# Optimization experiments

Measured on AMD Instinct MI355X. Metric: run time of the kernel, lower is better.

The kernel has to match this reference:

```python
import jax, jax.numpy as jnp
import numpy as np

H, W = 480, 640
TREF = 1.0        # reference timestamp (events warped to end of window)
TS_SCALING = 1.0  # width of timestamp normalization window
# 4 bilinear corner offsets (dy, dx): top-left, top-right, bottom-left, bottom-right
OFFS = np.array([[0.0, 0.0], [0.0, 1.0], [1.0, 0.0], [1.0, 1.0]], dtype=np.float32)


def setup_inputs() -> dict:
    key = jax.random.key(0)
    k1, k2, k3, k4, k5 = jax.random.split(key, 5)
    B, N = 4, 300000
    flow = jax.random.normal(k1, (B, 2, H, W), jnp.float32) * 2.0  # (x, y) flow maps
    ts = jax.random.uniform(k2, (B, N, 1), jnp.float32)            # event timestamps in [0,1]
    ev_y = jax.random.randint(k3, (B, N), 0, H)
    ev_x = jax.random.randint(k4, (B, N), 0, W)
    pol = jax.random.randint(k5, (B, N), 0, 2)                     # 1 = positive, 0 = negative
    return {"flow": flow, "ts": ts, "ev_y": ev_y, "ev_x": ev_x, "pol": pol}


def _corners(ev):
    """ev: [B,N,2] float (y,x) -> idx [B,4,N,2] corner coords, w [B,4,N] bilinear weights.
    Mirrors get_interpolation(): 4 integer corners, weights clamp(1-|d|,0,1) per axis."""
    base = jnp.floor(ev)[:, None, :, :]                      # [B,1,N,2]
    idx = base + jnp.asarray(OFFS)[None, :, None, :]          # [B,4,N,2]
    w = jnp.prod(jnp.clip(1.0 - jnp.abs(ev[:, None, :, :] - idx), 0.0, 1.0), axis=-1)
    return idx, w


def _splat(idx, w, pol_mask):
    """Mirrors interpolate(): masked bilinear scatter-add into a [B,1,H,W] image.
    idx: [B,4,N,2], w: [B,4,N], pol_mask: [B,1,N] (broadcast over 4 corners)."""
    B = idx.shape[0]
    inb = ((idx[..., 0] >= 0) & (idx[..., 0] <= H - 1) &
           (idx[..., 1] >= 0) & (idx[..., 1] <= W - 1)).astype(w.dtype)
    iy = jnp.clip(idx[..., 0], 0, H - 1).astype(jnp.int32)
    ix = jnp.clip(idx[..., 1], 0, W - 1).astype(jnp.int32)
    flat = (iy * W + ix).reshape(B, -1)                       # [B,4N]
    vals = (w * pol_mask * inb).reshape(B, -1)                # [B,4N]
    img = jnp.zeros((B, H * W), w.dtype).at[jnp.arange(B)[:, None], flat].add(vals)
    return img.reshape(B, 1, H, W)


def _sample(fmap, locs):
    """Mirrors get_event_flow(): bilinear gather of fmap [B,H,W] at float locs [B,N,2] (y,x)."""
    B = fmap.shape[0]
    idx, w = _corners(locs)
    inb = ((idx[..., 0] >= 0) & (idx[..., 0] <= H - 1) &
           (idx[..., 1] >= 0) & (idx[..., 1] <= W - 1)).astype(w.dtype)
    iy = jnp.clip(idx[..., 0], 0, H - 1).astype(jnp.int32)
    ix = jnp.clip(idx[..., 1], 0, W - 1).astype(jnp.int32)
    vals = fmap[jnp.arange(B)[:, None, None], iy, ix] * w * inb   # [B,4,N]
    return vals.sum(axis=1)                                        # [B,N]


def reference(flow, ts, ev_y, ev_x, pol):
    # event pixel locations (y, x)
    loc = jnp.stack([ev_y.astype(flow.dtype), ev_x.astype(flow.dtype)], axis=-1)  # [B,N,2]
    # gather per-event flow (flow channel 0 = x, channel 1 = y)
    fx = _sample(flow[:, 0], loc)   # [B,N]
    fy = _sample(flow[:, 1], loc)   # [B,N]
    # linear forward warp to tref
    dt = TREF - ts[..., 0]                                           # [B,N]
    warped = loc + dt[..., None] * jnp.stack([fy, fx], axis=-1)      # [B,N,2] (y,x)
    # iwe_formatting: bilinear splat of counts and normalized timestamps per polarity
    idx, w = _corners(warped)
    norm_ts = 1.0 - jnp.abs(TREF - ts[..., 0]) / TS_SCALING          # [B,N]
    pm_pos = (pol == 1).astype(w.dtype)[:, None, :]                  # [B,1,N]
    pm_neg = (pol == 0).astype(w.dtype)[:, None, :]
    iwe_pos = _splat(idx, w, pm_pos)
    iwe_neg = _splat(idx, w, pm_neg)
    wt = w * norm_ts[:, None, :]
    iwe_pos_ts = _splat(idx, wt, pm_pos)
    iwe_neg_ts = _splat(idx, wt, pm_neg)
    # [B,4,H,W]: (iwe_pos, iwe_neg, iwe_pos_ts, iwe_neg_ts)
    return jnp.concatenate([iwe_pos, iwe_neg, iwe_pos_ts, iwe_neg_ts], axis=1)
```

## Files before the change

kernel.cpp:

```cpp
#include <hip/hip_runtime.h>


#define IMG_H 480
#define IMG_W 640

#define OT_H 32
#define OT_W 32
#define OTY (IMG_H / OT_H)
#define OTX (IMG_W / OT_W)
#define OT_PER_B (OTY * OTX)
#define NB 4
#define NT (NB * OT_PER_B)

#define ACC_PLANE (OT_H * OT_W)

#define CURS_STRIDE 16
#define WS_CURS 0
#define WS_SPILLCNT 76800
#define WS_SPILL 81920
#define SPILL_CAP 32768
#define WS_RECS 606208

#define K1_THREADS 256
#define K1_IPT 8
#define K1_CHUNK (K1_THREADS * K1_IPT)

#define DUP_INVALID 0xFFFFFFFFu

#define QSCALE 1024.0f
#define INV_QSCALE 9.765625e-04f

#define Q20 1048576.0f
#define INV_Q20 9.5367431640625e-07f

__global__ void __launch_bounds__(K1_THREADS)
warp_scatter_kernel(const float* __restrict__ flow, const float* __restrict__ ts,
                    const int* __restrict__ ev_y, const int* __restrict__ ev_x,
                    const int* __restrict__ pol,
                    unsigned* __restrict__ dcurs, unsigned* __restrict__ spillcnt,
                    float4* __restrict__ spill, uint2* __restrict__ drecs,
                    int N, int cap, int nchunk) {
    __shared__ unsigned lh[OT_PER_B];
    __shared__ unsigned lbase[OT_PER_B];
    const int tid = threadIdx.x;
    const int L = blockIdx.x;
    const int b = (L >> 1) & 3;
    const int chunk = (L >> 3) * 2 + (L & 1);
    if (chunk >= nchunk) return;
    const int base = chunk * K1_CHUNK;

    for (int j = tid; j < OT_PER_B; j += K1_THREADS) lh[j] = 0;

    int   eyK[K1_IPT], exK[K1_IPT], poK[K1_IPT];
    float tsK[K1_IPT];
    bool  vK[K1_IPT];
    #pragma unroll
    for (int k = 0; k < K1_IPT; ++k) {
        const int idx = base + k * K1_THREADS + tid;
        vK[k] = (idx < N);
        const int i = b * N + (vK[k] ? idx : 0);
        eyK[k] = ev_y[i];
        exK[k] = ev_x[i];
        tsK[k] = ts[i];
        poK[k] = pol[i];
    }

    const float* fb = flow + (size_t)b * 2 * IMG_H * IMG_W;
    float fxK[K1_IPT], fyK[K1_IPT];
    #pragma unroll
    for (int k = 0; k < K1_IPT; ++k) {
        const int pix = eyK[k] * IMG_W + exK[k];
        fxK[k] = fb[pix];
        fyK[k] = fb[IMG_H * IMG_W + pix];
    }

    __syncthreads();

    float wyK[K1_IPT], wxK[K1_IPT];
    unsigned metaK[K1_IPT];
    unsigned dupS[K1_IPT][4];

    #pragma unroll
    for (int k = 0; k < K1_IPT; ++k) {
        float wy = 0.f, wx = 0.f;
        unsigned meta = 0;
        unsigned d0 = DUP_INVALID, d1 = DUP_INVALID,
                 d2 = DUP_INVALID, d3 = DUP_INVALID;
        if (vK[k]) {
            const float t = tsK[k];
            const float dt = 1.0f - t;
            wy = (float)eyK[k] + dt * fyK[k];
            wx = (float)exK[k] + dt * fxK[k];
            const float nts = 1.0f - fabsf(1.0f - t);
            const int p = poK[k] & 1;
            int qt = __float2int_rn(nts * 32767.0f);
            qt = min(max(qt, 0), 32767);
            meta = (unsigned)qt | ((unsigned)p << 15);

            const int iy0 = (int)floorf(wy);
            const int ix0 = (int)floorf(wx);
            const int ry0 = iy0 >> 5;
            const int ry1 = (iy0 + 1) >> 5;
            const bool cy0 = (iy0 >= 0) && (iy0 < IMG_H);
            const bool cy1 = (iy0 + 1 >= 0) && (iy0 + 1 < IMG_H)
                             && (!cy0 || ry1 != ry0);
            const int rx0 = ix0 >> 5;
            const int rx1 = (ix0 + 1) >> 5;
            const bool cx0 = (ix0 >= 0) && (ix0 < IMG_W);
            const bool cx1 = (ix0 + 1 >= 0) && (ix0 + 1 < IMG_W)
                             && (!cx0 || rx1 != rx0);

            if (cy0 && cx0) {
                const unsigned lt = (unsigned)(ry0 * OTX + rx0);
                d0 = (lt << 16) | atomicAdd(&lh[lt], 1u);
            }
            if (cy0 && cx1) {
                const unsigned lt = (unsigned)(ry0 * OTX + rx1);
                d1 = (lt << 16) | atomicAdd(&lh[lt], 1u);
            }
            if (cy1 && cx0) {
                const unsigned lt = (unsigned)(ry1 * OTX + rx0);
                d2 = (lt << 16) | atomicAdd(&lh[lt], 1u);
            }
            if (cy1 && cx1) {
                const unsigned lt = (unsigned)(ry1 * OTX + rx1);
                d3 = (lt << 16) | atomicAdd(&lh[lt], 1u);
            }
        }
        wyK[k] = wy; wxK[k] = wx; metaK[k] = meta;
        dupS[k][0] = d0; dupS[k][1] = d1; dupS[k][2] = d2; dupS[k][3] = d3;
    }
    __syncthreads();

    for (int j = tid; j < OT_PER_B; j += K1_THREADS) {
        const unsigned n = lh[j];
        lbase[j] = n ? atomicAdd(&dcurs[(size_t)(b * OT_PER_B + j) * CURS_STRIDE], n)
                     : 0u;
    }
    __syncthreads();

    #pragma unroll
    for (int k = 0; k < K1_IPT; ++k) {
        #pragma unroll
        for (int d = 0; d < 4; ++d) {
            const unsigned dp = dupS[k][d];
            if (dp == DUP_INVALID) continue;
            const unsigned lt = dp >> 16;
            const unsigned rk = dp & 0xFFFFu;
            const int dty = (int)(lt / OTX);
            const int dtx = (int)(lt % OTX);
            const unsigned slot = lbase[lt] + rk;
            if (slot < (unsigned)cap) {
                int qy = __float2int_rn((wyK[k] - 32.0f * dty + 1.0f) * QSCALE);
                int qx = __float2int_rn((wxK[k] - 32.0f * dtx + 1.0f) * QSCALE);
                qy = min(max(qy, 0), 65535);
                qx = min(max(qx, 0), 65535);
                uint2 dr;
                dr.x = (unsigned)qy | ((unsigned)qx << 16);
                dr.y = metaK[k];
                drecs[(size_t)(b * OT_PER_B + lt) * cap + slot] = dr;
            } else {
                const unsigned g = atomicAdd(spillcnt, 1u);
                if (g < SPILL_CAP) {
                    float4 s;
                    s.x = wyK[k]; s.y = wxK[k];
                    s.z = (float)(metaK[k] & 0x7FFFu) * (1.0f / 32767.0f);
                    s.w = __uint_as_float(0x80000000u
                            | (unsigned)((b << 1) | (metaK[k] >> 15))
                            | ((unsigned)dty << 8) | ((unsigned)dtx << 16));
                    spill[g] = s;
                }
            }
        }
    }
}

__device__ __forceinline__ void
splat_rec(unsigned rx_, unsigned ry_, unsigned long long* __restrict__ acc64) {
    const float ry  = (float)(rx_ & 0xFFFFu) * INV_QSCALE - 1.0f;
    const float rx  = (float)(rx_ >> 16)     * INV_QSCALE - 1.0f;
    const float nts = (float)(ry_ & 0x7FFFu) * (1.0f / 32767.0f);
    const int p = (int)((ry_ >> 15) & 1u);
    const float byf = floorf(ry), bxf = floorf(rx);
    const int iy0 = (int)byf, ix0 = (int)bxf;
    const float ay = ry - byf, ax = rx - bxf;
    const float wyv[2] = {1.0f - ay, ay};
    const float wxv[2] = {1.0f - ax, ax};
    unsigned long long* accp = acc64 + (p ? 0 : 1) * ACC_PLANE;
    #pragma unroll
    for (int dy = 0; dy < 2; ++dy) {
        const int gy = iy0 + dy;
        if ((unsigned)gy >= (unsigned)OT_H) continue;
        #pragma unroll
        for (int dx = 0; dx < 2; ++dx) {
            const int gx = ix0 + dx;
            if ((unsigned)gx >= (unsigned)OT_W) continue;
            const float w = wyv[dy] * wxv[dx];
            const unsigned qw  = __float2uint_rn(w * Q20);
            const unsigned qwt = __float2uint_rn(w * nts * Q20);
            atomicAdd(&accp[gy * OT_W + gx],
                      ((unsigned long long)qwt << 32) | (unsigned long long)qw);
        }
    }
}

__global__ void __launch_bounds__(256)
splat_kernel(const uint2* __restrict__ drecs, const unsigned* __restrict__ dcurs,
             const float4* __restrict__ spill, const unsigned* __restrict__ spillcnt,
             float* __restrict__ out, int cap) {
    __shared__ unsigned long long acc64[2 * ACC_PLANE];
    const int L = blockIdx.x;
    const int myb = (L >> 1) & 3;
    const int rb  = (L >> 3) * 2 + (L & 1);
    const int tile = myb * OT_PER_B + rb;
    const int tid = threadIdx.x;
    #pragma unroll
    for (int j = tid; j < 2 * ACC_PLANE; j += 256) acc64[j] = 0ull;
    __syncthreads();

    const int sy  = rb / OTX;
    const int sx  = rb % OTX;

    const unsigned cnt = min(dcurs[(size_t)tile * CURS_STRIDE], (unsigned)cap);
    const uint2* recs = drecs + (size_t)tile * cap;
    const uint4* base4 = (const uint4*)recs;
    const unsigned npair = cnt >> 1;
    for (unsigned u = tid; u < npair; u += 256) {
        const uint4 q = base4[u];
        splat_rec(q.x, q.y, acc64);
        splat_rec(q.z, q.w, acc64);
    }
    if ((cnt & 1u) && tid == 0) {
        const uint2 r = recs[cnt - 1];
        splat_rec(r.x, r.y, acc64);
    }

    const unsigned nsp = min(*spillcnt, (unsigned)SPILL_CAP);
    for (unsigned i = tid; i < nsp; i += 256) {
        const float4 s = spill[i];
        const unsigned meta = __float_as_uint(s.w);
        if ((int)((meta >> 1) & 3u) != myb) continue;
        if (meta & 0x80000000u) {
            if ((int)((meta >> 8) & 31u) != sy || (int)((meta >> 16) & 31u) != sx)
                continue;
        }
        const int p = (int)(meta & 1u);
        const float wy = s.x, wx = s.y, nts = s.z;
        const float byf = floorf(wy), bxf = floorf(wx);
        const int iy0 = (int)byf, ix0 = (int)bxf;
        const float ay = wy - byf, ax = wx - bxf;
        const float wyv[2] = {1.0f - ay, ay};
        const float wxv[2] = {1.0f - ax, ax};
        unsigned long long* accp = acc64 + (p ? 0 : 1) * ACC_PLANE;
        #pragma unroll
        for (int dy = 0; dy < 2; ++dy) {
            const int gy = iy0 + dy;
            if ((gy >> 5) != sy) continue;
            #pragma unroll
            for (int dx = 0; dx < 2; ++dx) {
                const int gx = ix0 + dx;
                if ((gx >> 5) != sx) continue;
                const float w = wyv[dy] * wxv[dx];
                const unsigned qw  = __float2uint_rn(w * Q20);
                const unsigned qwt = __float2uint_rn(w * nts * Q20);
                atomicAdd(&accp[(gy & 31) * OT_W + (gx & 31)],
                          ((unsigned long long)qwt << 32) | (unsigned long long)qw);
            }
        }
    }
    __syncthreads();

    const int y0 = sy * OT_H;
    const int x0 = sx * OT_W;
    float* outb = out + (size_t)myb * 4 * IMG_H * IMG_W;
    for (int q = tid; q < 2 * (ACC_PLANE / 4); q += 256) {
        const int pl  = q / (ACC_PLANE / 4);
        const int rem = q % (ACC_PLANE / 4);
        const int ry  = rem / (OT_W / 4);
        const int rx4 = rem % (OT_W / 4);
        float4 c4, t4;
        const unsigned long long* cell = acc64 + pl * ACC_PLANE + rem * 4;
        float* c = &c4.x; float* t = &t4.x;
        #pragma unroll
        for (int j = 0; j < 4; ++j) {
            const unsigned long long v = cell[j];
            c[j] = (float)(unsigned)(v & 0xFFFFFFFFull) * INV_Q20;
            t[j] = (float)(unsigned)(v >> 32) * INV_Q20;
        }
        const size_t off = (size_t)(y0 + ry) * IMG_W + x0 + rx4 * 4;
        *(float4*)(outb + (size_t)pl * IMG_H * IMG_W + off) = c4;
        *(float4*)(outb + (size_t)(pl + 2) * IMG_H * IMG_W + off) = t4;
    }
}

__device__ __forceinline__ void
warp_from(const float* __restrict__ flow, int b, int y, int x, float t,
          float& wy, float& wx, float& nts) {
    const float* fb = flow + (size_t)b * 2 * IMG_H * IMG_W;
    const int pix = y * IMG_W + x;
    const float fx = fb[pix];
    const float fy = fb[IMG_H * IMG_W + pix];
    const float dt = 1.0f - t;
    wy = (float)y + dt * fy;
    wx = (float)x + dt * fx;
    nts = 1.0f - fabsf(1.0f - t);
}

__global__ void __launch_bounds__(256)
event_splat_fallback(const float* __restrict__ flow, const float* __restrict__ ts,
                     const int* __restrict__ ev_y, const int* __restrict__ ev_x,
                     const int* __restrict__ pol, float* __restrict__ out,
                     int N, int total) {
    const int i = blockIdx.x * blockDim.x + threadIdx.x;
    if (i >= total) return;
    const int b = i / N;
    float wy, wx, nts;
    warp_from(flow, b, ev_y[i], ev_x[i], ts[i], wy, wx, nts);
    const int p = pol[i];
    const float byf = floorf(wy), bxf = floorf(wx);
    const int iy0 = (int)byf, ix0 = (int)bxf;
    const float ay = wy - byf, ax = wx - bxf;
    const float wyv[2] = {1.0f - ay, ay};
    const float wxv[2] = {1.0f - ax, ax};
    float* out_c = out + ((size_t)b * 4 + (p ? 0 : 1)) * IMG_H * IMG_W;
    float* out_t = out_c + 2 * IMG_H * IMG_W;
    #pragma unroll
    for (int dy = 0; dy < 2; ++dy) {
        const int gy = iy0 + dy;
        if (gy < 0 || gy >= IMG_H) continue;
        #pragma unroll
        for (int dx = 0; dx < 2; ++dx) {
            const int gx = ix0 + dx;
            if (gx < 0 || gx >= IMG_W) continue;
            const float w = wyv[dy] * wxv[dx];
            const int o = gy * IMG_W + gx;
            atomicAdd(out_c + o, w);
            atomicAdd(out_t + o, w * nts);
        }
    }
}

extern "C" void kernel_launch(void* const* d_in, const int* in_sizes, int n_in,
                              void* d_out, int out_size, void* d_ws, size_t ws_size,
                              hipStream_t stream) {
    const float* flow = (const float*)d_in[0];
    const float* ts   = (const float*)d_in[1];
    const int*   ev_y = (const int*)d_in[2];
    const int*   ev_x = (const int*)d_in[3];
    const int*   pol  = (const int*)d_in[4];
    float* out = (float*)d_out;

    const int total = in_sizes[2];
    const int B = out_size / (4 * IMG_H * IMG_W);
    const int N = total / B;
    char* ws = (char*)d_ws;

    int cap = 0;
    if (ws_size > (size_t)WS_RECS)
        cap = (int)((ws_size - WS_RECS) / ((size_t)NT * 8));
    if (cap > 4096) cap = 4096;
    cap &= ~3;

    if (B == NB && cap >= 1280) {
        unsigned* dcurs    = (unsigned*)(ws + WS_CURS);
        unsigned* spillcnt = (unsigned*)(ws + WS_SPILLCNT);
        float4*   spill    = (float4*)(ws + WS_SPILL);
        uint2*    drecs    = (uint2*)(ws + WS_RECS);

        hipMemsetAsync(ws, 0, WS_SPILL, stream);

        const int nchunk = (N + K1_CHUNK - 1) / K1_CHUNK;
        const int g1 = 8 * ((nchunk + 1) / 2);
        warp_scatter_kernel<<<g1, K1_THREADS, 0, stream>>>(
            flow, ts, ev_y, ev_x, pol, dcurs, spillcnt, spill, drecs,
            N, cap, nchunk);
        splat_kernel<<<NT, 256, 0, stream>>>(drecs, dcurs, spill, spillcnt,
                                             out, cap);
        return;
    }

    hipMemsetAsync(d_out, 0, (size_t)out_size * sizeof(float), stream);
    const int blocks = (total + 255) / 256;
    event_splat_fallback<<<blocks, 256, 0, stream>>>(flow, ts, ev_y, ev_x, pol,
                                                     out, N, total);
}
```

Baseline: 119.1 us.

## Fuse warp-scatter and splat passes into one cooperative kernel with grid sync

The two-kernel pipeline (event warp/bin scatter, then per-tile splat) becomes a single cooperative launch of 1024 blocks. A grid-wide sync separates the phases, and blocks then loop over the 1200 output tiles. The aim is to remove the second kernel launch and the gap between kernels. In exchange it adds grid-sync cost and a residency requirement (256 threads, 4 blocks per CU via launch bounds). Tiles no longer map one-to-one to blocks, so some blocks process two tiles serially. The old two-kernel path remains as a fallback if cooperative launch is unavailable or fails.

```diff
diff --git a/kernel.cpp b/kernel.cpp
--- a/kernel.cpp
+++ b/kernel.cpp
@@ -1,4 +1,7 @@
 #include <hip/hip_runtime.h>
+#include <hip/hip_cooperative_groups.h>
+
+namespace cg = cooperative_groups;
 
 
 #define IMG_H 480
@@ -25,6 +28,8 @@
 #define K1_IPT 8
 #define K1_CHUNK (K1_THREADS * K1_IPT)
 
+#define COOP_GRID 1024
+
 #define DUP_INVALID 0xFFFFFFFFu
 
 #define QSCALE 1024.0f
@@ -33,20 +38,14 @@
 #define Q20 1048576.0f
 #define INV_Q20 9.5367431640625e-07f
 
-__global__ void __launch_bounds__(K1_THREADS)
-warp_scatter_kernel(const float* __restrict__ flow, const float* __restrict__ ts,
-                    const int* __restrict__ ev_y, const int* __restrict__ ev_x,
-                    const int* __restrict__ pol,
-                    unsigned* __restrict__ dcurs, unsigned* __restrict__ spillcnt,
-                    float4* __restrict__ spill, uint2* __restrict__ drecs,
-                    int N, int cap, int nchunk) {
-    __shared__ unsigned lh[OT_PER_B];
-    __shared__ unsigned lbase[OT_PER_B];
-    const int tid = threadIdx.x;
-    const int L = blockIdx.x;
-    const int b = (L >> 1) & 3;
-    const int chunk = (L >> 3) * 2 + (L & 1);
-    if (chunk >= nchunk) return;
+__device__ __forceinline__ void
+k1_phase(const float* __restrict__ flow, const float* __restrict__ ts,
+         const int* __restrict__ ev_y, const int* __restrict__ ev_x,
+         const int* __restrict__ pol,
+         unsigned* __restrict__ dcurs, unsigned* __restrict__ spillcnt,
+         float4* __restrict__ spill, uint2* __restrict__ drecs,
+         int N, int cap, int b, int chunk, int tid,
+         unsigned* __restrict__ lh, unsigned* __restrict__ lbase) {
     const int base = chunk * K1_CHUNK;
 
     for (int j = tid; j < OT_PER_B; j += K1_THREADS) lh[j] = 0;
@@ -204,17 +203,15 @@
     }
 }
 
-__global__ void __launch_bounds__(256)
-splat_kernel(const uint2* __restrict__ drecs, const unsigned* __restrict__ dcurs,
-             const float4* __restrict__ spill, const unsigned* __restrict__ spillcnt,
-             float* __restrict__ out, int cap) {
-    __shared__ unsigned long long acc64[2 * ACC_PLANE];
-    const int L = blockIdx.x;
-    const int myb = (L >> 1) & 3;
-    const int rb  = (L >> 3) * 2 + (L & 1);
+__device__ __forceinline__ void
+k2_tile(const uint2* __restrict__ drecs, const unsigned* __restrict__ dcurs,
+        const float4* __restrict__ spill, const unsigned* __restrict__ spillcnt,
+        float* __restrict__ out, int cap, int t, int tid,
+        unsigned long long* __restrict__ acc64) {
+    const int myb = (t >> 1) & 3;
+    const int rb  = (t >> 3) * 2 + (t & 1);
     const int tile = myb * OT_PER_B + rb;
-    const int tid = threadIdx.x;
-    #pragma unroll
+
     for (int j = tid; j < 2 * ACC_PLANE; j += 256) acc64[j] = 0ull;
     __syncthreads();
 
@@ -280,17 +277,73 @@
         const int rx4 = rem % (OT_W / 4);
         float4 c4, t4;
         const unsigned long long* cell = acc64 + pl * ACC_PLANE + rem * 4;
-        float* c = &c4.x; float* t = &t4.x;
+        float* c = &c4.x; float* tt = &t4.x;
         #pragma unroll
         for (int j = 0; j < 4; ++j) {
             const unsigned long long v = cell[j];
-            c[j] = (float)(unsigned)(v & 0xFFFFFFFFull) * INV_Q20;
-            t[j] = (float)(unsigned)(v >> 32) * INV_Q20;
+            c[j]  = (float)(unsigned)(v & 0xFFFFFFFFull) * INV_Q20;
+            tt[j] = (float)(unsigned)(v >> 32) * INV_Q20;
         }
         const size_t off = (size_t)(y0 + ry) * IMG_W + x0 + rx4 * 4;
         *(float4*)(outb + (size_t)pl * IMG_H * IMG_W + off) = c4;
         *(float4*)(outb + (size_t)(pl + 2) * IMG_H * IMG_W + off) = t4;
     }
+    __syncthreads();
+}
+
+__global__ void __launch_bounds__(256, 4)
+fused_warp_splat(const float* __restrict__ flow, const float* __restrict__ ts,
+                 const int* __restrict__ ev_y, const int* __restrict__ ev_x,
+                 const int* __restrict__ pol,
+                 unsigned* __restrict__ dcurs, unsigned* __restrict__ spillcnt,
+                 float4* __restrict__ spill, uint2* __restrict__ drecs,
+                 float* __restrict__ out, int N, int cap, int nchunk) {
+    __shared__ unsigned long long acc64[2 * ACC_PLANE];
+    unsigned* lh    = (unsigned*)acc64;
+    unsigned* lbase = lh + OT_PER_B;
+
+    const int tid = threadIdx.x;
+    const int L = blockIdx.x;
+    const int b = (L >> 1) & 3;
+    const int chunk = (L >> 3) * 2 + (L & 1);
+
+    if (chunk < nchunk) {
+        k1_phase(flow, ts, ev_y, ev_x, pol, dcurs, spillcnt, spill, drecs,
+                 N, cap, b, chunk, tid, lh, lbase);
+    }
+
+    __threadfence();
+    cg::this_grid().sync();
+
+    for (int t = L; t < NT; t += (int)gridDim.x)
+        k2_tile(drecs, dcurs, spill, spillcnt, out, cap, t, tid, acc64);
+}
+
+__global__ void __launch_bounds__(K1_THREADS)
+warp_scatter_kernel(const float* __restrict__ flow, const float* __restrict__ ts,
+                    const int* __restrict__ ev_y, const int* __restrict__ ev_x,
+                    const int* __restrict__ pol,
+                    unsigned* __restrict__ dcurs, unsigned* __restrict__ spillcnt,
+                    float4* __restrict__ spill, uint2* __restrict__ drecs,
+                    int N, int cap, int nchunk) {
+    __shared__ unsigned lh[OT_PER_B];
+    __shared__ unsigned lbase[OT_PER_B];
+    const int tid = threadIdx.x;
+    const int L = blockIdx.x;
+    const int b = (L >> 1) & 3;
+    const int chunk = (L >> 3) * 2 + (L & 1);
+    if (chunk >= nchunk) return;
+    k1_phase(flow, ts, ev_y, ev_x, pol, dcurs, spillcnt, spill, drecs,
+             N, cap, b, chunk, tid, lh, lbase);
+}
+
+__global__ void __launch_bounds__(256)
+splat_kernel(const uint2* __restrict__ drecs, const unsigned* __restrict__ dcurs,
+             const float4* __restrict__ spill, const unsigned* __restrict__ spillcnt,
+             float* __restrict__ out, int cap) {
+    __shared__ unsigned long long acc64[2 * ACC_PLANE];
+    k2_tile(drecs, dcurs, spill, spillcnt, out, cap, blockIdx.x, threadIdx.x,
+            acc64);
 }
 
 __device__ __forceinline__ void
@@ -370,12 +423,34 @@
         hipMemsetAsync(ws, 0, WS_SPILL, stream);
 
         const int nchunk = (N + K1_CHUNK - 1) / K1_CHUNK;
-        const int g1 = 8 * ((nchunk + 1) / 2);
-        warp_scatter_kernel<<<g1, K1_THREADS, 0, stream>>>(
-            flow, ts, ev_y, ev_x, pol, dcurs, spillcnt, spill, drecs,
-            N, cap, nchunk);
-        splat_kernel<<<NT, 256, 0, stream>>>(drecs, dcurs, spill, spillcnt,
-                                             out, cap);
+
+        bool fused_ok = false;
+        {
+            int coop = 0, dev = 0;
+            if (hipGetDevice(&dev) == hipSuccess &&
+                hipDeviceGetAttribute(&coop, hipDeviceAttributeCooperativeLaunch,
+                                      dev) == hipSuccess && coop) {
+                void* args[] = {(void*)&flow, (void*)&ts, (void*)&ev_y,
+                                (void*)&ev_x, (void*)&pol, (void*)&dcurs,
+                                (void*)&spillcnt, (void*)&spill, (void*)&drecs,
+                                (void*)&out, (void*)&N, (void*)&cap,
+                                (void*)&nchunk};
+                if (hipLaunchCooperativeKernel((void*)fused_warp_splat,
+                                               dim3(COOP_GRID),
+                                               dim3(K1_THREADS),
+                                               args, 0, stream) == hipSuccess)
+                    fused_ok = true;
+            }
+        }
+
+        if (!fused_ok) {
+            const int g1 = 8 * ((nchunk + 1) / 2);
+            warp_scatter_kernel<<<g1, K1_THREADS, 0, stream>>>(
+                flow, ts, ev_y, ev_x, pol, dcurs, spillcnt, spill, drecs,
+                N, cap, nchunk);
+            splat_kernel<<<NT, 256, 0, stream>>>(drecs, dcurs, spill, spillcnt,
+                                                 out, cap);
+        }
         return;
     }
 
```

Result: slower. 373.9 us (+214.0%).
